# Kernel optimization log

Measured on AMD Instinct MI355X. Metric: run time of the kernel, lower is better.

Reference implementation:

```python
import jax, jax.numpy as jnp
import numpy as np

N_NODES = 100000
N_EDGES = 800000
IN_DIM, HID_DIM, OUT_DIM = 128, 256, 40


def setup_inputs() -> dict:
    key = jax.random.key(0)
    ks = jax.random.split(key, 8)
    x = jax.random.normal(ks[0], (N_NODES, IN_DIM), dtype=jnp.float32)
    edge_index = jax.random.randint(ks[1], (2, N_EDGES), 0, N_NODES, dtype=jnp.int64)
    # PyG SAGEConv params: lin_l (neighbor path, with bias), lin_r (root path, no bias)
    def glorot(k, fan_in, fan_out):
        lim = np.sqrt(6.0 / (fan_in + fan_out)).astype(np.float32)
        return jax.random.uniform(k, (fan_in, fan_out), jnp.float32, -lim, lim)
    W1l = glorot(ks[2], IN_DIM, HID_DIM)
    W1r = glorot(ks[3], IN_DIM, HID_DIM)
    b1 = jnp.zeros((HID_DIM,), jnp.float32)
    W2l = glorot(ks[4], HID_DIM, OUT_DIM)
    W2r = glorot(ks[5], HID_DIM, OUT_DIM)
    b2 = jnp.zeros((OUT_DIM,), jnp.float32)
    return {"x": x, "edge_index": edge_index, "W1l": W1l, "b1": b1, "W1r": W1r,
            "W2l": W2l, "b2": b2, "W2r": W2r}


def _sage_conv(x, src, dst, Wl, b, Wr, n_nodes):
    # mean aggregation of neighbor features: gather x[src], scatter-add to dst, divide by degree
    msg = x[src]                                              # [E, D]
    agg = jax.ops.segment_sum(msg, dst, num_segments=n_nodes)  # [N, D]
    cnt = jax.ops.segment_sum(jnp.ones((src.shape[0],), x.dtype), dst,
                              num_segments=n_nodes)            # [N]
    agg = agg / jnp.maximum(cnt, 1.0)[:, None]
    # out = lin_l(mean_agg) + lin_r(x)  (lin_l carries the bias in PyG)
    return agg @ Wl + b + x @ Wr


def reference(x, edge_index, W1l, b1, W1r, W2l, b2, W2r):
    src, dst = edge_index[0], edge_index[1]
    n = x.shape[0]
    h = _sage_conv(x, src, dst, W1l, b1, W1r, n)
    h = jax.nn.relu(h)
    # F.dropout(training=self.training): identity at inference
    out = _sage_conv(h, src, dst, W2l, b2, W2r, n)
    return out
```

## Files before the change

### kernel.cpp

```cpp
#include <hip/hip_runtime.h>
#include <hip/hip_bf16.h>


#define NN   100000
#define NNP  100096
#define NE   800000
#define NB1  391
#define NCHK 32
#define ECH  25000
#define NSLI 16
#define NSL  6250

typedef unsigned short ushortT;
typedef __attribute__((ext_vector_type(8))) short bf16x8;
typedef __attribute__((ext_vector_type(4))) float f32x4;

__device__ __forceinline__ unsigned short f2b(float f) {
    unsigned u = __float_as_uint(f);
    return (unsigned short)((u + 0x7fffu + ((u >> 16) & 1u)) >> 16);
}
__device__ __forceinline__ float b2f(unsigned short v) {
    return __uint_as_float(((unsigned)v) << 16);
}
__device__ __forceinline__ void llds16(const unsigned short* g, unsigned short* s) {
    __builtin_amdgcn_global_load_lds(
        (const __attribute__((address_space(1))) void*)g,
        (__attribute__((address_space(3))) void*)s, 16, 0, 0);
}
__device__ __forceinline__ int fragIdx(int n, int k) {
    return (((n >> 4) * 8 + (k >> 5)) * 64 + ((k >> 3) & 3) * 16 + (n & 15)) * 8
           + (k & 7);
}

__global__ __launch_bounds__(256) void k_prep(
        const float* __restrict__ x,
        const float* __restrict__ W1l, const float* __restrict__ W1r,
        const float* __restrict__ W2l, const float* __restrict__ W2r,
        ushortT* __restrict__ Ac, ushortT* __restrict__ WT1f,
        ushortT* __restrict__ WT2f,
        const int* __restrict__ dst, int* __restrict__ deg32) {
    __shared__ int hist[NSL];
    int bid = blockIdx.x;
    if (bid < 12500) {
        int t = bid * 256 + threadIdx.x;
        int row = t >> 5, c4 = t & 31;
        float4 v = *(const float4*)&x[(size_t)row * 128 + c4 * 4];
        ushort4 o;
        o.x = f2b(v.x); o.y = f2b(v.y); o.z = f2b(v.z); o.w = f2b(v.w);
        *(ushort4*)(Ac + (size_t)row * 256 + 128 + c4 * 4) = o;

        if (t < 65536) {
            int n = t >> 8, k = t & 255;
            float w = (k < 128) ? W1l[(size_t)k * 256 + n]
                                : W1r[(size_t)(k - 128) * 256 + n];
            WT1f[fragIdx(n, k)] = f2b(w);
        } else if (t < 65536 + 20480) {
            int j = t - 65536;
            int n = j >> 8, k = j & 255;
            float w = (n < 40) ? W2l[(size_t)k * 40 + n]
                               : W2r[(size_t)k * 40 + (n - 40)];
            WT2f[fragIdx(n, k)] = f2b(w);
        }
    } else {
        int idx = bid - 12500;
        int s = idx & (NSLI - 1), c = idx >> 4;
        for (int i = threadIdx.x; i < NSL; i += 256) hist[i] = 0;
        __syncthreads();
        int e0 = c * ECH, lo = s * NSL;
        for (int i = threadIdx.x; i < ECH; i += 1024) {
            int d[4];
            bool m[4];
#pragma unroll
            for (int u = 0; u < 4; ++u) {
                int ii = i + u * 256;
                m[u] = ii < ECH;
                d[u] = dst[e0 + (m[u] ? ii : 0)];
            }
#pragma unroll
            for (int u = 0; u < 4; ++u) {
                unsigned dd = (unsigned)(d[u] - lo);
                if (m[u] && dd < (unsigned)NSL) atomicAdd(&hist[dd], 1);
            }
        }
        __syncthreads();
        for (int i = threadIdx.x; i < NSL; i += 256)
            deg32[c * NN + lo + i] = hist[i];
    }
}

__global__ __launch_bounds__(256) void k_scan1(const int* __restrict__ deg32,
                                               int* __restrict__ rp,
                                               int* __restrict__ rpp,
                                               int* __restrict__ bsum) {
    __shared__ int s[256];
    int t = threadIdx.x;
    int i = blockIdx.x * 256 + t;
    int d32[NCHK];
    int v = 0;
#pragma unroll
    for (int r = 0; r < NCHK; ++r) {
        d32[r] = (i < NN) ? deg32[r * NN + i] : 0;
        v += d32[r];
    }
    s[t] = v;
    __syncthreads();
    for (int off = 1; off < 256; off <<= 1) {
        int add = (t >= off) ? s[t - off] : 0;
        __syncthreads();
        s[t] += add;
        __syncthreads();
    }
    int ex = s[t] - v;
    if (i <= NN) rp[i] = ex;
    if (i < NN) {
        int run = ex;
#pragma unroll
        for (int r = 0; r < NCHK; ++r) {
            rpp[r * NN + i] = run;
            run += d32[r];
        }
    }
    if (t == 255) bsum[blockIdx.x] = s[255];
}

__global__ __launch_bounds__(512) void k_scan2(int* __restrict__ bsum) {
    __shared__ int s[512];
    int t = threadIdx.x;
    int v = (t < NB1) ? bsum[t] : 0;
    s[t] = v;
    __syncthreads();
    for (int off = 1; off < 512; off <<= 1) {
        int add = (t >= off) ? s[t - off] : 0;
        __syncthreads();
        s[t] += add;
        __syncthreads();
    }
    if (t < NB1) bsum[t] = s[t] - v;
}

__global__ __launch_bounds__(256) void k_fillB(const int* __restrict__ src,
                                               const int* __restrict__ dst,
                                               const int* __restrict__ rpp,
                                               const int* __restrict__ bsum,
                                               int* __restrict__ col) {
    __shared__ int off[NSL];
    int s = blockIdx.x & (NSLI - 1), c = blockIdx.x >> 4;
    int lo = s * NSL;
    for (int i = threadIdx.x; i < NSL; i += 256)
        off[i] = bsum[(lo + i) >> 8] + rpp[c * NN + lo + i];
    __syncthreads();
    int e0 = c * ECH;
    for (int i = threadIdx.x; i < ECH; i += 1024) {
        int d[4], sv[4];
        bool m[4];
#pragma unroll
        for (int u = 0; u < 4; ++u) {
            int ii = i + u * 256;
            m[u] = ii < ECH;
            int e = e0 + (m[u] ? ii : 0);
            d[u] = dst[e];
            sv[u] = src[e];
        }
#pragma unroll
        for (int u = 0; u < 4; ++u) {
            unsigned dd = (unsigned)(d[u] - lo);
            if (m[u] && dd < (unsigned)NSL) {
                int k = atomicAdd(&off[dd], 1);
                col[k] = sv[u];
            }
        }
    }
}

__global__ __launch_bounds__(256) void k_agg1(const int* __restrict__ rp,
                                              const int* __restrict__ bsum,
                                              const int* __restrict__ col,
                                              ushortT* __restrict__ Ac) {
    int node = blockIdx.x * 4 + (threadIdx.x >> 6);
    int l = threadIdx.x & 63;
    if (node >= NN) return;
    int seg = l >> 4, dl = l & 15;
    int beg = rp[node] + bsum[node >> 8];
    int end = rp[node + 1] + bsum[(node + 1) >> 8];
    int deg = end - beg;
    float a[8] = {0.f, 0.f, 0.f, 0.f, 0.f, 0.f, 0.f, 0.f};
    for (int base = 0; base < deg; base += 64) {
        int cnt = min(64, deg - base);
        int cv = col[beg + base + min(l, cnt - 1)];
        for (int j = 0; j < cnt; j += 16) {
            int e[4], idx[4];
            bf16x8 v[4];
#pragma unroll
            for (int u = 0; u < 4; ++u) {
                e[u] = j + u * 4 + seg;
                idx[u] = __shfl(cv, min(e[u], cnt - 1));
            }
#pragma unroll
            for (int u = 0; u < 4; ++u) {
                v[u] = (bf16x8){0, 0, 0, 0, 0, 0, 0, 0};
                if (e[u] < cnt)
                    v[u] = *(const bf16x8*)(Ac + (size_t)idx[u] * 256 + 128 + dl * 8);
            }
#pragma unroll
            for (int u = 0; u < 4; ++u)
#pragma unroll
                for (int i = 0; i < 8; ++i)
                    a[i] += b2f((unsigned short)v[u][i]);
        }
    }
#pragma unroll
    for (int i = 0; i < 8; ++i) {
        a[i] += __shfl_xor(a[i], 16);
        a[i] += __shfl_xor(a[i], 32);
    }
    if (seg == 0) {
        float inv = 1.0f / fmaxf((float)deg, 1.0f);
        bf16x8 o;
#pragma unroll
        for (int i = 0; i < 8; ++i) o[i] = (short)f2b(a[i] * inv);
        *(bf16x8*)(Ac + (size_t)node * 256 + dl * 8) = o;
    }
}

#define HSP 264
__global__ __launch_bounds__(512, 3) void k_fused(
        const ushortT* __restrict__ Ac, const ushortT* __restrict__ WT1f,
        const float* __restrict__ b1, const ushortT* __restrict__ WT2f,
        const float* __restrict__ b2, ushortT* __restrict__ y2,
        ushortT* __restrict__ t) {
    __shared__ ushortT Bs[64 * HSP];
    const int tid = threadIdx.x, l = tid & 63, wid = tid >> 6;
    const int m0 = blockIdx.x * 64;
    const int q = l >> 4, r = l & 15;
    const int swz = (l & 7) ^ ((l >> 3) & 7);

#pragma unroll
    for (int i = 0; i < 4; ++i) {
        int idx = wid * 4 + i;
        int ktc = idx >> 3, flat = idx & 7;
        int row = flat * 8 + (l >> 3);
        llds16(Ac + (size_t)(m0 + row) * 256 + ktc * 64 + swz * 8,
               &Bs[ktc * 4096 + flat * 512]);
    }

    const ushortT* bBase = WT1f + (size_t)(wid * 16) * 512 + l * 8;
    bf16x8 bfr[16];
#pragma unroll
    for (int kc = 0; kc < 8; ++kc)
#pragma unroll
        for (int nt = 0; nt < 2; ++nt)
            bfr[kc * 2 + nt] = *(const bf16x8*)(bBase + (size_t)(nt * 8 + kc) * 512);

    float bb1[2];
#pragma unroll
    for (int nt = 0; nt < 2; ++nt) bb1[nt] = b1[wid * 32 + nt * 16 + r];

    f32x4 acc[4][2];
#pragma unroll
    for (int i = 0; i < 4; ++i)
#pragma unroll
        for (int j = 0; j < 2; ++j) acc[i][j] = (f32x4){0.f, 0.f, 0.f, 0.f};

    __syncthreads();

#pragma unroll
    for (int kc = 0; kc < 8; ++kc) {
        const int ktc = kc >> 1, ks = (kc & 1) * 32;
        const int cs = (((ks >> 3) + q) ^ (r & 7)) * 8;
        bf16x8 af[4];
#pragma unroll
        for (int mt = 0; mt < 4; ++mt)
            af[mt] = *(const bf16x8*)&Bs[ktc * 4096 + (mt * 16 + r) * 64 + cs];
#pragma unroll
        for (int mt = 0; mt < 4; ++mt)
#pragma unroll
            for (int nt = 0; nt < 2; ++nt)
                acc[mt][nt] = __builtin_amdgcn_mfma_f32_16x16x32_bf16(
                    af[mt], bfr[kc * 2 + nt], acc[mt][nt], 0, 0, 0);
    }

    bf16x8 bq[8];
    float bb2 = 0.f;
    if (wid < 5) {
#pragma unroll
        for (int kc = 0; kc < 8; ++kc)
            bq[kc] = *(const bf16x8*)(WT2f + (size_t)(wid * 8 + kc) * 512 + l * 8);
        int c = wid * 16 + r;
        if (c >= 40) bb2 = b2[c - 40];
    }

    __syncthreads();

#pragma unroll
    for (int nt = 0; nt < 2; ++nt) {
        int colb = wid * 32 + nt * 16 + r;
#pragma unroll
        for (int mt = 0; mt < 4; ++mt) {
            int rowb = mt * 16 + q * 4;
#pragma unroll
            for (int j = 0; j < 4; ++j)
                Bs[(rowb + j) * HSP + colb] =
                    f2b(fmaxf(acc[mt][nt][j] + bb1[nt], 0.f));
        }
    }
    __syncthreads();

    if (wid < 5) {
        f32x4 acc2[4];
#pragma unroll
        for (int j = 0; j < 4; ++j) acc2[j] = (f32x4){0.f, 0.f, 0.f, 0.f};
#pragma unroll
        for (int kc = 0; kc < 8; ++kc) {
            bf16x8 af2[4];
#pragma unroll
            for (int mt = 0; mt < 4; ++mt)
                af2[mt] = *(const bf16x8*)&Bs[(mt * 16 + r) * HSP + kc * 32 + q * 8];
#pragma unroll
            for (int mt = 0; mt < 4; ++mt)
                acc2[mt] = __builtin_amdgcn_mfma_f32_16x16x32_bf16(
                    af2[mt], bq[kc], acc2[mt], 0, 0, 0);
        }
        int c = wid * 16 + r;
#pragma unroll
        for (int mt = 0; mt < 4; ++mt) {
            int row0 = m0 + mt * 16 + q * 4;
#pragma unroll
            for (int j = 0; j < 4; ++j) {
                float v = acc2[mt][j];
                if (c < 40)
                    y2[(size_t)(row0 + j) * 40 + c] = f2b(v);
                else
                    t[(size_t)(row0 + j) * 40 + (c - 40)] = f2b(v + bb2);
            }
        }
    }
}

__global__ __launch_bounds__(256) void k_agg2(const int* __restrict__ rp,
                                              const int* __restrict__ bsum,
                                              const int* __restrict__ col,
                                              const ushortT* __restrict__ y2,
                                              const ushortT* __restrict__ t,
                                              float* __restrict__ out) {
    int node = blockIdx.x * 4 + (threadIdx.x >> 6);
    int l = threadIdx.x & 63;
    if (node >= NN) return;
    int seg = l >> 4, dl = l & 15;
    int beg = rp[node] + bsum[node >> 8];
    int end = rp[node + 1] + bsum[(node + 1) >> 8];
    int deg = end - beg;
    bool act = dl < 10;
    float a0 = 0.f, a1 = 0.f, a2 = 0.f, a3 = 0.f;
    for (int base = 0; base < deg; base += 64) {
        int cnt = min(64, deg - base);
        int cv = col[beg + base + min(l, cnt - 1)];
        for (int j = 0; j < cnt; j += 16) {
            int e[4], idx[4];
            ushort4 v[4];
#pragma unroll
            for (int u = 0; u < 4; ++u) {
                e[u] = j + u * 4 + seg;
                idx[u] = __shfl(cv, min(e[u], cnt - 1));
            }
#pragma unroll
            for (int u = 0; u < 4; ++u) {
                v[u] = (ushort4){0, 0, 0, 0};
                if (e[u] < cnt && act)
                    v[u] = *(const ushort4*)(y2 + (size_t)idx[u] * 40 + dl * 4);
            }
#pragma unroll
            for (int u = 0; u < 4; ++u) {
                a0 += b2f(v[u].x);
                a1 += b2f(v[u].y);
                a2 += b2f(v[u].z);
                a3 += b2f(v[u].w);
            }
        }
    }
    a0 += __shfl_xor(a0, 16); a0 += __shfl_xor(a0, 32);
    a1 += __shfl_xor(a1, 16); a1 += __shfl_xor(a1, 32);
    a2 += __shfl_xor(a2, 16); a2 += __shfl_xor(a2, 32);
    a3 += __shfl_xor(a3, 16); a3 += __shfl_xor(a3, 32);
    if (seg == 0 && act) {
        float inv = 1.0f / fmaxf((float)deg, 1.0f);
        size_t o = (size_t)node * 40 + dl * 4;
        ushort4 tv = *(const ushort4*)&t[o];
        float4 ov;
        ov.x = a0 * inv + b2f(tv.x);
        ov.y = a1 * inv + b2f(tv.y);
        ov.z = a2 * inv + b2f(tv.z);
        ov.w = a3 * inv + b2f(tv.w);
        *(float4*)&out[o] = ov;
    }
}

extern "C" void kernel_launch(void* const* d_in, const int* in_sizes, int n_in,
                              void* d_out, int out_size, void* d_ws, size_t ws_size,
                              hipStream_t stream) {
    const float* x   = (const float*)d_in[0];
    const int*   ei  = (const int*)d_in[1];
    const int*   src = ei;
    const int*   dst = ei + NE;
    const float* W1l = (const float*)d_in[2];
    const float* b1  = (const float*)d_in[3];
    const float* W1r = (const float*)d_in[4];
    const float* W2l = (const float*)d_in[5];
    const float* b2  = (const float*)d_in[6];
    const float* W2r = (const float*)d_in[7];
    float* out = (float*)d_out;

    size_t off = 0;
    char* base = (char*)d_ws;
    auto alloc = [&](size_t bytes) -> void* {
        void* p = base + off;
        off += (bytes + 255) & ~(size_t)255;
        return p;
    };
    int*     deg32 = (int*)alloc((size_t)NCHK * NN * 4);
    int*     rp    = (int*)alloc((size_t)(NN + 1) * 4);
    int*     rpp   = (int*)alloc((size_t)NCHK * NN * 4);
    int*     col   = (int*)alloc((size_t)NE * 4);
    int*     bsum  = (int*)alloc(512 * 4);
    ushortT* Ac    = (ushortT*)alloc((size_t)NNP * 256 * 2);
    ushortT* y2    = (ushortT*)alloc((size_t)NNP * 40 * 2);
    ushortT* t     = (ushortT*)alloc((size_t)NNP * 40 * 2);
    ushortT* WT1f  = (ushortT*)alloc(256 * 256 * 2);
    ushortT* WT2f  = (ushortT*)alloc(80 * 256 * 2);

    k_prep<<<12500 + NCHK * NSLI, 256, 0, stream>>>(x, W1l, W1r, W2l, W2r,
                                                    Ac, WT1f, WT2f, dst, deg32);
    k_scan1<<<NB1, 256, 0, stream>>>(deg32, rp, rpp, bsum);
    k_scan2<<<1, 512, 0, stream>>>(bsum);
    k_fillB<<<NCHK * NSLI, 256, 0, stream>>>(src, dst, rpp, bsum, col);
    k_agg1<<<(NN + 3) / 4, 256, 0, stream>>>(rp, bsum, col, Ac);
    k_fused<<<NNP / 64, 512, 0, stream>>>(Ac, WT1f, b1, WT2f, b2, y2, t);
    k_agg2<<<(NN + 3) / 4, 256, 0, stream>>>(rp, bsum, col, y2, t, out);
}
```

Baseline: 263.4 us.

## Fuse layer-1 neighbor aggregation into the fused GEMM kernel via LDS

Removes the separate k_agg1 kernel and computes the mean aggregation of neighbor features inside k_fused. Each wave aggregates 8 nodes and writes the result straight into the swizzled LDS A-tile. The bf16 x copy shrinks to a 128-wide buffer with no aggregated half. This drops one kernel launch plus the global write and re-read of the aggregated features. The cost is that the latency-bound gather now runs inside a GEMM kernel with lower occupancy (launch bounds 512,3), so the gathers may be poorly hidden.

```diff
diff --git a/kernel.cpp b/kernel.cpp
--- a/kernel.cpp
+++ b/kernel.cpp
@@ -36,7 +36,7 @@
         const float* __restrict__ x,
         const float* __restrict__ W1l, const float* __restrict__ W1r,
         const float* __restrict__ W2l, const float* __restrict__ W2r,
-        ushortT* __restrict__ Ac, ushortT* __restrict__ WT1f,
+        ushortT* __restrict__ Xb, ushortT* __restrict__ WT1f,
         ushortT* __restrict__ WT2f,
         const int* __restrict__ dst, int* __restrict__ deg32) {
     __shared__ int hist[NSL];
@@ -47,7 +47,7 @@
         float4 v = *(const float4*)&x[(size_t)row * 128 + c4 * 4];
         ushort4 o;
         o.x = f2b(v.x); o.y = f2b(v.y); o.z = f2b(v.z); o.w = f2b(v.w);
-        *(ushort4*)(Ac + (size_t)row * 256 + 128 + c4 * 4) = o;
+        *(ushort4*)(Xb + (size_t)row * 128 + c4 * 4) = o;
 
         if (t < 65536) {
             int n = t >> 8, k = t & 255;
@@ -172,62 +172,13 @@
     }
 }
 
-__global__ __launch_bounds__(256) void k_agg1(const int* __restrict__ rp,
-                                              const int* __restrict__ bsum,
-                                              const int* __restrict__ col,
-                                              ushortT* __restrict__ Ac) {
-    int node = blockIdx.x * 4 + (threadIdx.x >> 6);
-    int l = threadIdx.x & 63;
-    if (node >= NN) return;
-    int seg = l >> 4, dl = l & 15;
-    int beg = rp[node] + bsum[node >> 8];
-    int end = rp[node + 1] + bsum[(node + 1) >> 8];
-    int deg = end - beg;
-    float a[8] = {0.f, 0.f, 0.f, 0.f, 0.f, 0.f, 0.f, 0.f};
-    for (int base = 0; base < deg; base += 64) {
-        int cnt = min(64, deg - base);
-        int cv = col[beg + base + min(l, cnt - 1)];
-        for (int j = 0; j < cnt; j += 16) {
-            int e[4], idx[4];
-            bf16x8 v[4];
-#pragma unroll
-            for (int u = 0; u < 4; ++u) {
-                e[u] = j + u * 4 + seg;
-                idx[u] = __shfl(cv, min(e[u], cnt - 1));
-            }
-#pragma unroll
-            for (int u = 0; u < 4; ++u) {
-                v[u] = (bf16x8){0, 0, 0, 0, 0, 0, 0, 0};
-                if (e[u] < cnt)
-                    v[u] = *(const bf16x8*)(Ac + (size_t)idx[u] * 256 + 128 + dl * 8);
-            }
-#pragma unroll
-            for (int u = 0; u < 4; ++u)
-#pragma unroll
-                for (int i = 0; i < 8; ++i)
-                    a[i] += b2f((unsigned short)v[u][i]);
-        }
-    }
-#pragma unroll
-    for (int i = 0; i < 8; ++i) {
-        a[i] += __shfl_xor(a[i], 16);
-        a[i] += __shfl_xor(a[i], 32);
-    }
-    if (seg == 0) {
-        float inv = 1.0f / fmaxf((float)deg, 1.0f);
-        bf16x8 o;
-#pragma unroll
-        for (int i = 0; i < 8; ++i) o[i] = (short)f2b(a[i] * inv);
-        *(bf16x8*)(Ac + (size_t)node * 256 + dl * 8) = o;
-    }
-}
-
 #define HSP 264
 __global__ __launch_bounds__(512, 3) void k_fused(
-        const ushortT* __restrict__ Ac, const ushortT* __restrict__ WT1f,
-        const float* __restrict__ b1, const ushortT* __restrict__ WT2f,
-        const float* __restrict__ b2, ushortT* __restrict__ y2,
-        ushortT* __restrict__ t) {
+        const ushortT* __restrict__ Xb, const int* __restrict__ rp,
+        const int* __restrict__ bsum, const int* __restrict__ col,
+        const ushortT* __restrict__ WT1f, const float* __restrict__ b1,
+        const ushortT* __restrict__ WT2f, const float* __restrict__ b2,
+        ushortT* __restrict__ y2, ushortT* __restrict__ t) {
     __shared__ ushortT Bs[64 * HSP];
     const int tid = threadIdx.x, l = tid & 63, wid = tid >> 6;
     const int m0 = blockIdx.x * 64;
@@ -235,11 +186,11 @@
     const int swz = (l & 7) ^ ((l >> 3) & 7);
 
 #pragma unroll
-    for (int i = 0; i < 4; ++i) {
-        int idx = wid * 4 + i;
-        int ktc = idx >> 3, flat = idx & 7;
+    for (int i = 0; i < 2; ++i) {
+        int idx = wid * 2 + i;
+        int ktc = 2 + (idx >> 3), flat = idx & 7;
         int row = flat * 8 + (l >> 3);
-        llds16(Ac + (size_t)(m0 + row) * 256 + ktc * 64 + swz * 8,
+        llds16(Xb + (size_t)(m0 + row) * 128 + (ktc - 2) * 64 + swz * 8,
                &Bs[ktc * 4096 + flat * 512]);
     }
 
@@ -254,6 +205,58 @@
     float bb1[2];
 #pragma unroll
     for (int nt = 0; nt < 2; ++nt) bb1[nt] = b1[wid * 32 + nt * 16 + r];
+
+    {
+        const int seg = l >> 4, dl = l & 15;
+        for (int n = 0; n < 8; ++n) {
+            int node = m0 + wid * 8 + n;
+            float a[8] = {0.f, 0.f, 0.f, 0.f, 0.f, 0.f, 0.f, 0.f};
+            int deg = 0;
+            if (node < NN) {
+                int beg = rp[node] + bsum[node >> 8];
+                int end = rp[node + 1] + bsum[(node + 1) >> 8];
+                deg = end - beg;
+                for (int base = 0; base < deg; base += 64) {
+                    int cnt = min(64, deg - base);
+                    int cv = col[beg + base + min(l, cnt - 1)];
+                    for (int j = 0; j < cnt; j += 16) {
+                        int e[4], idx[4];
+                        bf16x8 v[4];
+#pragma unroll
+                        for (int u = 0; u < 4; ++u) {
+                            e[u] = j + u * 4 + seg;
+                            idx[u] = __shfl(cv, min(e[u], cnt - 1));
+                        }
+#pragma unroll
+                        for (int u = 0; u < 4; ++u) {
+                            v[u] = (bf16x8){0, 0, 0, 0, 0, 0, 0, 0};
+                            if (e[u] < cnt)
+                                v[u] = *(const bf16x8*)(Xb + (size_t)idx[u] * 128 + dl * 8);
+                        }
+#pragma unroll
+                        for (int u = 0; u < 4; ++u)
+#pragma unroll
+                            for (int i = 0; i < 8; ++i)
+                                a[i] += b2f((unsigned short)v[u][i]);
+                    }
+                }
+            }
+#pragma unroll
+            for (int i = 0; i < 8; ++i) {
+                a[i] += __shfl_xor(a[i], 16);
+                a[i] += __shfl_xor(a[i], 32);
+            }
+            if (seg == 0) {
+                float inv = 1.0f / fmaxf((float)deg, 1.0f);
+                bf16x8 o;
+#pragma unroll
+                for (int i = 0; i < 8; ++i) o[i] = (short)f2b(a[i] * inv);
+                int widx = (dl >> 3) * 4096 + wid * 512
+                         + (n * 8 + ((dl ^ n) & 7)) * 8;
+                *(bf16x8*)&Bs[widx] = o;
+            }
+        }
+    }
 
     f32x4 acc[4][2];
 #pragma unroll
@@ -421,18 +424,18 @@
     int*     rpp   = (int*)alloc((size_t)NCHK * NN * 4);
     int*     col   = (int*)alloc((size_t)NE * 4);
     int*     bsum  = (int*)alloc(512 * 4);
-    ushortT* Ac    = (ushortT*)alloc((size_t)NNP * 256 * 2);
+    ushortT* Xb    = (ushortT*)alloc((size_t)NNP * 128 * 2);
     ushortT* y2    = (ushortT*)alloc((size_t)NNP * 40 * 2);
     ushortT* t     = (ushortT*)alloc((size_t)NNP * 40 * 2);
     ushortT* WT1f  = (ushortT*)alloc(256 * 256 * 2);
     ushortT* WT2f  = (ushortT*)alloc(80 * 256 * 2);
 
     k_prep<<<12500 + NCHK * NSLI, 256, 0, stream>>>(x, W1l, W1r, W2l, W2r,
-                                                    Ac, WT1f, WT2f, dst, deg32);
+                                                    Xb, WT1f, WT2f, dst, deg32);
     k_scan1<<<NB1, 256, 0, stream>>>(deg32, rp, rpp, bsum);
     k_scan2<<<1, 512, 0, stream>>>(bsum);
     k_fillB<<<NCHK * NSLI, 256, 0, stream>>>(src, dst, rpp, bsum, col);
-    k_agg1<<<(NN + 3) / 4, 256, 0, stream>>>(rp, bsum, col, Ac);
-    k_fused<<<NNP / 64, 512, 0, stream>>>(Ac, WT1f, b1, WT2f, b2, y2, t);
+    k_fused<<<NNP / 64, 512, 0, stream>>>(Xb, rp, bsum, col,
+                                          WT1f, b1, WT2f, b2, y2, t);
     k_agg2<<<(NN + 3) / 4, 256, 0, stream>>>(rp, bsum, col, y2, t, out);
 }
```

New measurement: 272.9 us. +3.6%, slower.
